# Performance work log

Hardware: AMD Instinct MI355X
Metric: run time of the kernel (lower is better)

Reference implementation:

```python
import jax, jax.numpy as jnp
import numpy as np

B, D = 64, 512          # batch, in_dims
P, PS, S = 128, 3, 64   # num_patches, patch_size, scene_size


def setup_inputs() -> dict:
    key = jax.random.key(0)
    k0, k1, k2, k3 = jax.random.split(key, 4)
    z = jax.random.normal(k0, (B, D), jnp.float32)
    Wm = jax.random.normal(k1, (P * PS * PS, D), jnp.float32) * 0.02
    bm = jnp.zeros((P * PS * PS,), jnp.float32)
    Wt = jax.random.normal(k2, (6 * P, D), jnp.float32) * 0.01
    # module initializes transform bias to [scale,0,0,0,scale,0] per patch (scale=2)
    bt = jnp.tile(jnp.array([2.0, 0.0, 0.0, 0.0, 2.0, 0.0], jnp.float32), P)
    noise = jax.random.normal(k3, (PS, PS), jnp.float32)
    return {"z": z, "Wm": Wm, "bm": bm, "Wt": Wt, "bt": bt, "noise": noise}


def _affine_grid(theta, size):
    # theta: (N,2,3). Matches torch affine_grid(align_corners=False).
    c = (jnp.arange(size, dtype=theta.dtype) + 0.5) / size * 2.0 - 1.0
    xg, yg = jnp.meshgrid(c, c)  # xg[h,w]=c[w], yg[h,w]=c[h]
    base = jnp.stack([xg, yg, jnp.ones_like(xg)], axis=-1)  # (S,S,3)
    return jnp.einsum('nij,hwj->nhwi', theta, base)  # (N,S,S,2), [...,0]=x, [...,1]=y


def _grid_sample_bilinear_zeros(img, grid):
    # img: (N,Hi,Wi), grid: (N,Ho,Wo,2). torch grid_sample bilinear, zeros padding,
    # align_corners=False.
    N, Hi, Wi = img.shape
    ix = ((grid[..., 0] + 1.0) * Wi - 1.0) * 0.5
    iy = ((grid[..., 1] + 1.0) * Hi - 1.0) * 0.5
    ix0 = jnp.floor(ix)
    iy0 = jnp.floor(iy)
    wx1 = ix - ix0
    wy1 = iy - iy0
    wx0 = 1.0 - wx1
    wy0 = 1.0 - wy1
    b = jnp.arange(N)[:, None, None]

    def gather(xf, yf):
        xi = xf.astype(jnp.int32)
        yi = yf.astype(jnp.int32)
        valid = (xi >= 0) & (xi < Wi) & (yi >= 0) & (yi < Hi)
        xc = jnp.clip(xi, 0, Wi - 1)
        yc = jnp.clip(yi, 0, Hi - 1)
        return jnp.where(valid, img[b, yc, xc], 0.0)

    v00 = gather(ix0, iy0)
    v01 = gather(ix0 + 1.0, iy0)
    v10 = gather(ix0, iy0 + 1.0)
    v11 = gather(ix0 + 1.0, iy0 + 1.0)
    return (wy0 * (wx0 * v00 + wx1 * v01) + wy1 * (wx0 * v10 + wx1 * v11))


def reference(z, Wm, bm, Wt, bt, noise):
    Bz = z.shape[0]
    # refine_patches=True path: masks = 1 - sigmoid(Linear(z))
    masks = 1.0 - jax.nn.sigmoid(z @ Wm.T + bm)
    masks = masks.reshape(Bz, P, PS, PS) * noise  # patch_noise multiply
    theta = (z @ Wt.T + bt).reshape(Bz, P, 2, 3)
    imgs = masks.reshape(Bz * P, PS, PS)
    th = theta.reshape(Bz * P, 2, 3)
    grid = _affine_grid(th, S)                      # (B*P, S, S, 2)
    out = _grid_sample_bilinear_zeros(imgs, grid)   # (B*P, S, S)
    return out.reshape(Bz, P, S, S)
```

## Files before the change

kernel.cpp:

```cpp
#include <hip/hip_runtime.h>
#include <math.h>

#define BATCH 64
#define DIM 512
#define NPATCH 128
#define SSZ 64

__global__ __launch_bounds__(256) void k_fused(
    const float* __restrict__ z, const float* __restrict__ Wm,
    const float* __restrict__ bm, const float* __restrict__ Wt,
    const float* __restrict__ bt, const float* __restrict__ noise,
    float* __restrict__ out) {
  __shared__ float sm[16];

  const int t = threadIdx.x;
  const int bp = blockIdx.x;
  const int b = bp >> 7;
  const int p = bp & 127;

  const int r = t >> 4;
  const int c = t & 15;
  float acc = 0.0f;
  if (r < 15) {
    const float* __restrict__ wrow =
        (r < 9) ? (Wm + (size_t)(p * 9 + r) * DIM)
                : (Wt + (size_t)(p * 6 + (r - 9)) * DIM);
    const float* __restrict__ zrow = z + (size_t)b * DIM;
#pragma unroll
    for (int i = 0; i < 8; ++i) {
      const float4 wv = *(const float4*)(wrow + i * 64 + c * 4);
      const float4 zv = *(const float4*)(zrow + i * 64 + c * 4);
      acc = fmaf(wv.x, zv.x, acc);
      acc = fmaf(wv.y, zv.y, acc);
      acc = fmaf(wv.z, zv.z, acc);
      acc = fmaf(wv.w, zv.w, acc);
    }
  }
  acc += __shfl_xor(acc, 1);
  acc += __shfl_xor(acc, 2);
  acc += __shfl_xor(acc, 4);
  acc += __shfl_xor(acc, 8);
  if (c == 0 && r < 15) {
    float v = acc;
    if (r < 9) {
      v = (1.0f / (1.0f + expf(v + bm[p * 9 + r]))) * noise[r];
    } else {
      v += bt[p * 6 + (r - 9)];
    }
    sm[r] = v;
  }
  __syncthreads();

  const float m00 = sm[0], m01 = sm[1], m02 = sm[2];
  const float m10 = sm[3], m11 = sm[4], m12 = sm[5];
  const float m20 = sm[6], m21 = sm[7], m22 = sm[8];
  const float th0 = sm[9], th1 = sm[10], th2 = sm[11];
  const float th3 = sm[12], th4 = sm[13], th5 = sm[14];

  const int w4 = (t & 15) << 2;
  const int hb = t >> 4;
  const float cx0 = (w4 + 0.5f) * (1.0f / 32.0f) - 1.0f;
  const float cy0 = (hb + 0.5f) * (1.0f / 32.0f) - 1.0f;
  const float dix = th0 * (1.5f / 32.0f);
  const float diy = th3 * (1.5f / 32.0f);
  const float Bx = 1.5f * th1, By = 1.5f * th4;
  const float Px = fmaf(1.5f, fmaf(th0, cx0, th2), 1.0f);
  const float Py = fmaf(1.5f, fmaf(th3, cx0, th5), 1.0f);

  float* op = out + ((size_t)bp << 12) + hb * 64 + w4;

#pragma unroll
  for (int i = 0; i < 4; ++i) {
    const float cy = cy0 + 0.5f * i;
    float ix = fmaf(Bx, cy, Px);
    float iy = fmaf(By, cy, Py);
    float4 rv;
    float* rp = &rv.x;
#pragma unroll
    for (int j = 0; j < 4; ++j) {
      const float wx0 = fmaxf(1.0f - fabsf(ix), 0.0f);
      const float wx1 = fmaxf(1.0f - fabsf(ix - 1.0f), 0.0f);
      const float wx2 = fmaxf(1.0f - fabsf(ix - 2.0f), 0.0f);
      const float wy0 = fmaxf(1.0f - fabsf(iy), 0.0f);
      const float wy1 = fmaxf(1.0f - fabsf(iy - 1.0f), 0.0f);
      const float wy2 = fmaxf(1.0f - fabsf(iy - 2.0f), 0.0f);
      const float s0 = fmaf(m02, wx2, fmaf(m01, wx1, m00 * wx0));
      const float s1 = fmaf(m12, wx2, fmaf(m11, wx1, m10 * wx0));
      const float s2 = fmaf(m22, wx2, fmaf(m21, wx1, m20 * wx0));
      rp[j] = fmaf(wy2, s2, fmaf(wy1, s1, wy0 * s0));
      ix += dix;
      iy += diy;
    }
    *(float4*)(op + i * 16 * 64) = rv;
  }
}

extern "C" void kernel_launch(void* const* d_in, const int* in_sizes, int n_in,
                              void* d_out, int out_size, void* d_ws, size_t ws_size,
                              hipStream_t stream) {
  const float* z     = (const float*)d_in[0];
  const float* Wm    = (const float*)d_in[1];
  const float* bm    = (const float*)d_in[2];
  const float* Wt    = (const float*)d_in[3];
  const float* bt    = (const float*)d_in[4];
  const float* noise = (const float*)d_in[5];
  float* out = (float*)d_out;

  hipLaunchKernelGGL(k_fused, dim3(BATCH * NPATCH), dim3(256), 0, stream,
                     z, Wm, bm, Wt, bt, noise, out);
}
```

Before: 161.0 us.

## Split fused kernel into batched GEMV with shared z tile and separate sampler

Replaces the single fused kernel with two launches. The first computes all mask and theta values per patch for 16 batch rows at once, staging z in padded shared memory so each weight row is read once per 16 batches. The second kernel reads those coefficients from workspace and renders the 64x64 patch, using fmed3 for the clamped tent weights and nontemporal stores for the output. The aim is to cut the redundant weight traffic, which in the fused kernel re-reads every weight row once per batch row. The cost is an extra launch and a workspace round trip, and the old fused path is kept as a fallback when no workspace is given.

```diff
diff --git a/kernel.cpp b/kernel.cpp
--- a/kernel.cpp
+++ b/kernel.cpp
@@ -5,6 +5,115 @@
 #define DIM 512
 #define NPATCH 128
 #define SSZ 64
+#define PADZ 516
+
+typedef float f32x4 __attribute__((ext_vector_type(4)));
+
+__global__ __launch_bounds__(256) void k_gemm(
+    const float* __restrict__ z, const float* __restrict__ Wm,
+    const float* __restrict__ bm, const float* __restrict__ Wt,
+    const float* __restrict__ bt, const float* __restrict__ noise,
+    float* __restrict__ ws) {
+  __shared__ float zs[16 * PADZ];
+  const int p = blockIdx.x;
+  const int bq = blockIdx.y;
+  const int t = threadIdx.x;
+
+  {
+    const f32x4* __restrict__ src = (const f32x4*)(z + (size_t)(bq * 16) * DIM);
+#pragma unroll
+    for (int i = 0; i < 8; ++i) {
+      const int idx = t + (i << 8);
+      const int row = idx >> 7;
+      const int col = idx & 127;
+      *(f32x4*)(zs + row * PADZ + (col << 2)) = src[idx];
+    }
+  }
+  __syncthreads();
+
+  const int r = t >> 4;
+  const int bl = t & 15;
+  if (r >= 15) return;
+
+  const float* __restrict__ wrow =
+      (r < 9) ? (Wm + (size_t)(p * 9 + r) * DIM)
+              : (Wt + (size_t)(p * 6 + (r - 9)) * DIM);
+  const float* __restrict__ zr = zs + bl * PADZ;
+
+  float a0 = 0.0f, a1 = 0.0f, a2 = 0.0f, a3 = 0.0f;
+#pragma unroll 8
+  for (int i = 0; i < 128; ++i) {
+    const f32x4 wv = ((const f32x4*)wrow)[i];
+    const f32x4 zv = *(const f32x4*)(zr + (i << 2));
+    a0 = fmaf(wv.x, zv.x, a0);
+    a1 = fmaf(wv.y, zv.y, a1);
+    a2 = fmaf(wv.z, zv.z, a2);
+    a3 = fmaf(wv.w, zv.w, a3);
+  }
+  const float acc = (a0 + a1) + (a2 + a3);
+
+  const int b = (bq << 4) + bl;
+  float v;
+  if (r < 9) {
+    v = (1.0f / (1.0f + expf(acc + bm[p * 9 + r]))) * noise[r];
+  } else {
+    v = acc + bt[p * 6 + (r - 9)];
+  }
+  ws[(((size_t)b << 7) + p) * 16 + r] = v;
+}
+
+__global__ __launch_bounds__(256) void k_sample(
+    const float* __restrict__ ws, float* __restrict__ out) {
+  __shared__ float sm[16];
+  const int t = threadIdx.x;
+  const int bp = blockIdx.x;
+  if (t < 16) sm[t] = ws[((size_t)bp << 4) + t];
+  __syncthreads();
+
+  const float m00 = sm[0], m01 = sm[1], m02 = sm[2];
+  const float m10 = sm[3], m11 = sm[4], m12 = sm[5];
+  const float m20 = sm[6], m21 = sm[7], m22 = sm[8];
+  const float th0 = sm[9], th1 = sm[10], th2 = sm[11];
+  const float th3 = sm[12], th4 = sm[13], th5 = sm[14];
+
+  const int w4 = (t & 15) << 2;
+  const int hb = t >> 4;
+  const float cx0 = (w4 + 0.5f) * (1.0f / 32.0f) - 1.0f;
+  const float cy0 = (hb + 0.5f) * (1.0f / 32.0f) - 1.0f;
+  const float dix = th0 * (1.5f / 32.0f);
+  const float diy = th3 * (1.5f / 32.0f);
+  const float Bx = 1.5f * th1, By = 1.5f * th4;
+  const float Px = fmaf(1.5f, fmaf(th0, cx0, th2), 1.0f);
+  const float Py = fmaf(1.5f, fmaf(th3, cx0, th5), 1.0f);
+
+  float* op = out + ((size_t)bp << 12) + hb * 64 + w4;
+
+#pragma unroll
+  for (int i = 0; i < 4; ++i) {
+    const float cy = cy0 + 0.5f * i;
+    const float ix = fmaf(Bx, cy, Px);
+    const float iy = fmaf(By, cy, Py);
+    float ax = ix + 1.0f, bx = 1.0f - ix;
+    float ay = iy + 1.0f, by = 1.0f - iy;
+    f32x4 rv;
+#pragma unroll
+    for (int j = 0; j < 4; ++j) {
+      const float wx0 = __builtin_amdgcn_fmed3f(0.0f, ax, bx);
+      const float wx1 = __builtin_amdgcn_fmed3f(0.0f, ax - 1.0f, bx + 1.0f);
+      const float wx2 = __builtin_amdgcn_fmed3f(0.0f, ax - 2.0f, bx + 2.0f);
+      const float wy0 = __builtin_amdgcn_fmed3f(0.0f, ay, by);
+      const float wy1 = __builtin_amdgcn_fmed3f(0.0f, ay - 1.0f, by + 1.0f);
+      const float wy2 = __builtin_amdgcn_fmed3f(0.0f, ay - 2.0f, by + 2.0f);
+      const float s0 = fmaf(m02, wx2, fmaf(m01, wx1, m00 * wx0));
+      const float s1 = fmaf(m12, wx2, fmaf(m11, wx1, m10 * wx0));
+      const float s2 = fmaf(m22, wx2, fmaf(m21, wx1, m20 * wx0));
+      rv[j] = fmaf(wy2, s2, fmaf(wy1, s1, wy0 * s0));
+      ax += dix; bx -= dix;
+      ay += diy; by -= diy;
+    }
+    __builtin_nontemporal_store(rv, (f32x4*)(op + i * 16 * 64));
+  }
+}
 
 __global__ __launch_bounds__(256) void k_fused(
     const float* __restrict__ z, const float* __restrict__ Wm,
@@ -106,6 +215,15 @@
   const float* noise = (const float*)d_in[5];
   float* out = (float*)d_out;
 
-  hipLaunchKernelGGL(k_fused, dim3(BATCH * NPATCH), dim3(256), 0, stream,
-                     z, Wm, bm, Wt, bt, noise, out);
-}
+  const size_t need = (size_t)BATCH * NPATCH * 16 * sizeof(float);
+  if (d_ws != nullptr && ws_size >= need) {
+    float* ws = (float*)d_ws;
+    hipLaunchKernelGGL(k_gemm, dim3(NPATCH, 4), dim3(256), 0, stream,
+                       z, Wm, bm, Wt, bt, noise, ws);
+    hipLaunchKernelGGL(k_sample, dim3(BATCH * NPATCH), dim3(256), 0, stream,
+                       ws, out);
+  } else {
+    hipLaunchKernelGGL(k_fused, dim3(BATCH * NPATCH), dim3(256), 0, stream,
+                       z, Wm, bm, Wt, bt, noise, out);
+  }
+}
```

Result: no change. 162.4 us (+0.9%).

## Process four patches per block with one wavefront per patch

Applied to the files above, without the earlier changes.

Each block now handles four patches instead of one. In the prologue, every 4-thread group computes a full 512-length dot product with four partial accumulators, so all 256 threads are busy instead of only 240 lanes each doing a 32-element slice. In the render phase each wavefront owns one patch: it broadcasts the 15 parameters by shuffle and writes 16 rows of float4s, and the tent weights are computed with fmed3. The aim is to amortise block launch and prologue latency over more output; the trade-off is a grid four times smaller and longer per-thread serial dot products.

```diff
diff --git a/kernel.cpp b/kernel.cpp
--- a/kernel.cpp
+++ b/kernel.cpp
@@ -6,92 +6,107 @@
 #define NPATCH 128
 #define SSZ 64
 
-__global__ __launch_bounds__(256) void k_fused(
+typedef float f32x4 __attribute__((ext_vector_type(4)));
+
+__global__ __launch_bounds__(256) void k_fused2(
     const float* __restrict__ z, const float* __restrict__ Wm,
     const float* __restrict__ bm, const float* __restrict__ Wt,
     const float* __restrict__ bt, const float* __restrict__ noise,
     float* __restrict__ out) {
-  __shared__ float sm[16];
+  __shared__ float sm[64];
 
   const int t = threadIdx.x;
-  const int bp = blockIdx.x;
-  const int b = bp >> 7;
-  const int p = bp & 127;
+  const int blk = blockIdx.x;
+  const int b = blk >> 5;
+  const int p0 = (blk & 31) << 2;
 
-  const int r = t >> 4;
-  const int c = t & 15;
-  float acc = 0.0f;
-  if (r < 15) {
+  {
+    const int s = t >> 2;
+    const int c = t & 3;
+    const int q = s >> 4;
+    const int r = s & 15;
+    const int rr = (r < 15) ? r : 14;
+    const int p = p0 + q;
+
     const float* __restrict__ wrow =
-        (r < 9) ? (Wm + (size_t)(p * 9 + r) * DIM)
-                : (Wt + (size_t)(p * 6 + (r - 9)) * DIM);
-    const float* __restrict__ zrow = z + (size_t)b * DIM;
-#pragma unroll
-    for (int i = 0; i < 8; ++i) {
-      const float4 wv = *(const float4*)(wrow + i * 64 + c * 4);
-      const float4 zv = *(const float4*)(zrow + i * 64 + c * 4);
-      acc = fmaf(wv.x, zv.x, acc);
-      acc = fmaf(wv.y, zv.y, acc);
-      acc = fmaf(wv.z, zv.z, acc);
-      acc = fmaf(wv.w, zv.w, acc);
+        (rr < 9) ? (Wm + (size_t)(p * 9 + rr) * DIM)
+                 : (Wt + (size_t)(p * 6 + (rr - 9)) * DIM);
+    const f32x4* __restrict__ wq = (const f32x4*)wrow + c;
+    const f32x4* __restrict__ zq = (const f32x4*)(z + (size_t)b * DIM) + c;
+
+    float a0 = 0.0f, a1 = 0.0f, a2 = 0.0f, a3 = 0.0f;
+#pragma unroll 8
+    for (int k = 0; k < 32; ++k) {
+      const f32x4 wv = wq[k << 2];
+      const f32x4 zv = zq[k << 2];
+      a0 = fmaf(wv.x, zv.x, a0);
+      a1 = fmaf(wv.y, zv.y, a1);
+      a2 = fmaf(wv.z, zv.z, a2);
+      a3 = fmaf(wv.w, zv.w, a3);
     }
-  }
-  acc += __shfl_xor(acc, 1);
-  acc += __shfl_xor(acc, 2);
-  acc += __shfl_xor(acc, 4);
-  acc += __shfl_xor(acc, 8);
-  if (c == 0 && r < 15) {
-    float v = acc;
-    if (r < 9) {
-      v = (1.0f / (1.0f + expf(v + bm[p * 9 + r]))) * noise[r];
-    } else {
-      v += bt[p * 6 + (r - 9)];
+    float acc = (a0 + a1) + (a2 + a3);
+    acc += __shfl_xor(acc, 1);
+    acc += __shfl_xor(acc, 2);
+
+    if (c == 0 && r < 15) {
+      float v;
+      if (r < 9) {
+        v = (1.0f / (1.0f + expf(acc + bm[p * 9 + r]))) * noise[r];
+      } else {
+        v = acc + bt[p * 6 + (r - 9)];
+      }
+      sm[s] = v;
     }
-    sm[r] = v;
   }
   __syncthreads();
 
-  const float m00 = sm[0], m01 = sm[1], m02 = sm[2];
-  const float m10 = sm[3], m11 = sm[4], m12 = sm[5];
-  const float m20 = sm[6], m21 = sm[7], m22 = sm[8];
-  const float th0 = sm[9], th1 = sm[10], th2 = sm[11];
-  const float th3 = sm[12], th4 = sm[13], th5 = sm[14];
+  const int w = t >> 6;
+  const int lane = t & 63;
 
-  const int w4 = (t & 15) << 2;
-  const int hb = t >> 4;
+  const float rec = sm[(w << 4) + (lane & 15)];
+  const float m00 = __shfl(rec, 0), m01 = __shfl(rec, 1), m02 = __shfl(rec, 2);
+  const float m10 = __shfl(rec, 3), m11 = __shfl(rec, 4), m12 = __shfl(rec, 5);
+  const float m20 = __shfl(rec, 6), m21 = __shfl(rec, 7), m22 = __shfl(rec, 8);
+  const float th0 = __shfl(rec, 9), th1 = __shfl(rec, 10), th2 = __shfl(rec, 11);
+  const float th3 = __shfl(rec, 12), th4 = __shfl(rec, 13), th5 = __shfl(rec, 14);
+
+  const int w4 = (lane & 15) << 2;
+  const int rsub = lane >> 4;
   const float cx0 = (w4 + 0.5f) * (1.0f / 32.0f) - 1.0f;
-  const float cy0 = (hb + 0.5f) * (1.0f / 32.0f) - 1.0f;
+  const float cy0 = (rsub + 0.5f) * (1.0f / 32.0f) - 1.0f;
   const float dix = th0 * (1.5f / 32.0f);
   const float diy = th3 * (1.5f / 32.0f);
-  const float Bx = 1.5f * th1, By = 1.5f * th4;
-  const float Px = fmaf(1.5f, fmaf(th0, cx0, th2), 1.0f);
-  const float Py = fmaf(1.5f, fmaf(th3, cx0, th5), 1.0f);
+  const float dAx = th1 * (1.5f * 0.125f);
+  const float dAy = th4 * (1.5f * 0.125f);
+  const float ixb0 = fmaf(1.5f, fmaf(th0, cx0, fmaf(th1, cy0, th2)), 1.0f);
+  const float iyb0 = fmaf(1.5f, fmaf(th3, cx0, fmaf(th4, cy0, th5)), 1.0f);
 
-  float* op = out + ((size_t)bp << 12) + hb * 64 + w4;
+  float* op = out + (((size_t)(blk << 2) + w) << 12) + (rsub << 6) + w4;
 
-#pragma unroll
-  for (int i = 0; i < 4; ++i) {
-    const float cy = cy0 + 0.5f * i;
-    float ix = fmaf(Bx, cy, Px);
-    float iy = fmaf(By, cy, Py);
-    float4 rv;
-    float* rp = &rv.x;
+#pragma unroll 2
+  for (int a = 0; a < 16; ++a) {
+    float ix = fmaf((float)a, dAx, ixb0);
+    float iy = fmaf((float)a, dAy, iyb0);
+    f32x4 rv;
 #pragma unroll
     for (int j = 0; j < 4; ++j) {
-      const float wx0 = fmaxf(1.0f - fabsf(ix), 0.0f);
-      const float wx1 = fmaxf(1.0f - fabsf(ix - 1.0f), 0.0f);
-      const float wx2 = fmaxf(1.0f - fabsf(ix - 2.0f), 0.0f);
-      const float wy0 = fmaxf(1.0f - fabsf(iy), 0.0f);
-      const float wy1 = fmaxf(1.0f - fabsf(iy - 1.0f), 0.0f);
-      const float wy2 = fmaxf(1.0f - fabsf(iy - 2.0f), 0.0f);
+      const float ax = ix + 1.0f, bx = 1.0f - ix;
+      const float ay = iy + 1.0f, by = 1.0f - iy;
+      const float wx0 = __builtin_amdgcn_fmed3f(0.0f, ax, bx);
+      const float wx1 = __builtin_amdgcn_fmed3f(0.0f, ax - 1.0f, bx + 1.0f);
+      const float wx2 = __builtin_amdgcn_fmed3f(0.0f, ax - 2.0f, bx + 2.0f);
+      const float wy0 = __builtin_amdgcn_fmed3f(0.0f, ay, by);
+      const float wy1 = __builtin_amdgcn_fmed3f(0.0f, ay - 1.0f, by + 1.0f);
+      const float wy2 = __builtin_amdgcn_fmed3f(0.0f, ay - 2.0f, by + 2.0f);
       const float s0 = fmaf(m02, wx2, fmaf(m01, wx1, m00 * wx0));
       const float s1 = fmaf(m12, wx2, fmaf(m11, wx1, m10 * wx0));
       const float s2 = fmaf(m22, wx2, fmaf(m21, wx1, m20 * wx0));
-      rp[j] = fmaf(wy2, s2, fmaf(wy1, s1, wy0 * s0));
+      rv[j] = fmaf(wy2, s2, fmaf(wy1, s1, wy0 * s0));
       ix += dix;
       iy += diy;
     }
-    *(float4*)(op + i * 16 * 64) = rv;
+    *(f32x4*)op = rv;
+    op += 256;
   }
 }
 
@@ -106,6 +121,6 @@
   const float* noise = (const float*)d_in[5];
   float* out = (float*)d_out;
 
-  hipLaunchKernelGGL(k_fused, dim3(BATCH * NPATCH), dim3(256), 0, stream,
+  hipLaunchKernelGGL(k_fused2, dim3(BATCH * NPATCH / 4), dim3(256), 0, stream,
                      z, Wm, bm, Wt, bt, noise, out);
 }
```

Result: no change. 160.9 us (-0.0%).
